# Optimization experiments

Hardware: AMD Instinct MI355X
Metric: run time of the kernel (lower is better)

Reference implementation:

```python
import jax, jax.numpy as jnp
import numpy as np

B, H, W, DIM, HEADS, WS = 32, 56, 56, 192, 6, 7
KD = DIM // HEADS          # key_dim = head_dim = 32 (attn_ratio=1.0 -> d = KD, dh = DIM)
DH = KD * HEADS
HQKV = DH + 2 * KD * HEADS # 576
L = H * W
HIDDEN = 4 * DIM
NWIN = (H // WS) * (W // WS)
NTOK = WS * WS
SCALE = KD ** -0.5


def _bias_idxs(ws):
    pts = [(i, j) for i in range(ws) for j in range(ws)]
    offs, idxs = {}, []
    for p1 in pts:
        for p2 in pts:
            o = (abs(p1[0] - p2[0]), abs(p1[1] - p2[1]))
            if o not in offs:
                offs[o] = len(offs)
            idxs.append(offs[o])
    return np.asarray(idxs, np.int32).reshape(ws * ws, ws * ws), len(offs)

BIAS_IDX, NOFF = _bias_idxs(WS)  # [49,49], 49 distinct offsets


def _ln(x, g, b, eps=1e-5):
    m = x.mean(-1, keepdims=True)
    v = jnp.mean((x - m) ** 2, -1, keepdims=True)
    return (x - m) * jax.lax.rsqrt(v + eps) * g + b


def setup_inputs() -> dict:
    key = jax.random.key(0)
    ks = jax.random.split(key, 8)
    f32 = jnp.float32
    return {
        "x": jax.random.normal(ks[0], (B, L, DIM), f32),
        "ln1_g": jnp.ones((DIM,), f32), "ln1_b": jnp.zeros((DIM,), f32),
        "qkv_w": jax.random.normal(ks[1], (DIM, HQKV), f32) * 0.02,
        "qkv_b": jnp.zeros((HQKV,), f32),
        "proj_w": jax.random.normal(ks[2], (DH, DIM), f32) * 0.02,
        "proj_b": jnp.zeros((DIM,), f32),
        "attn_bias": jax.random.normal(ks[3], (HEADS, NOFF), f32) * 0.02,
        "conv_w": jax.random.normal(ks[4], (DIM, 1, 3, 3), f32) * 0.1,  # depthwise OIHW
        "bn_g": jnp.ones((DIM,), f32), "bn_b": jnp.zeros((DIM,), f32),
        "bn_m": jnp.zeros((DIM,), f32), "bn_v": jnp.ones((DIM,), f32),
        "ln2_g": jnp.ones((DIM,), f32), "ln2_b": jnp.zeros((DIM,), f32),
        "fc1_w": jax.random.normal(ks[5], (DIM, HIDDEN), f32) * 0.02,
        "fc1_b": jnp.zeros((HIDDEN,), f32),
        "fc2_w": jax.random.normal(ks[6], (HIDDEN, DIM), f32) * 0.02,
        "fc2_b": jnp.zeros((DIM,), f32),
    }


def reference(x, ln1_g, ln1_b, qkv_w, qkv_b, proj_w, proj_b, attn_bias,
              conv_w, bn_g, bn_b, bn_m, bn_v, ln2_g, ln2_b,
              fc1_w, fc1_b, fc2_w, fc2_b):
    # ---- window partition: [B,L,C] -> [B*nWin, 49, C] (H,W divisible by WS, no pad)
    xw = x.reshape(B, H // WS, WS, W // WS, WS, DIM)
    xw = xw.transpose(0, 1, 3, 2, 4, 5).reshape(B * NWIN, NTOK, DIM)
    # ---- attention (pre-LN inside Attention module)
    h = _ln(xw, ln1_g, ln1_b)
    qkv = (h @ qkv_w + qkv_b).reshape(B * NWIN, NTOK, HEADS, 3 * KD)
    qkv = qkv.transpose(0, 2, 1, 3)                      # [Bw, heads, N, 3*KD]
    q, k, v = qkv[..., :KD], qkv[..., KD:2 * KD], qkv[..., 2 * KD:]
    bias = attn_bias[:, BIAS_IDX]                        # [heads, 49, 49] gathered table
    scores = jnp.einsum('bhnd,bhmd->bhnm', q, k) * SCALE + bias[None]
    a = jax.nn.softmax(scores, axis=-1)
    o = jnp.einsum('bhnm,bhmd->bhnd', a, v)
    o = o.transpose(0, 2, 1, 3).reshape(B * NWIN, NTOK, DH)
    o = o @ proj_w + proj_b
    # ---- window unpartition -> [B,L,C], residual add
    o = o.reshape(B, H // WS, W // WS, WS, WS, DIM)
    o = o.transpose(0, 1, 3, 2, 4, 5).reshape(B, L, DIM)
    x = x + o
    # ---- depthwise 3x3 conv + BN (eval-mode) in NCHW
    xc = x.transpose(0, 2, 1).reshape(B, DIM, H, W)
    xc = jax.lax.conv_general_dilated(
        xc, conv_w, window_strides=(1, 1), padding=[(1, 1), (1, 1)],
        feature_group_count=DIM, dimension_numbers=('NCHW', 'OIHW', 'NCHW'))
    inv = jax.lax.rsqrt(bn_v + 1e-5)
    xc = (xc - bn_m[None, :, None, None]) * (inv * bn_g)[None, :, None, None] + bn_b[None, :, None, None]
    x = xc.reshape(B, DIM, L).transpose(0, 2, 1)
    # ---- MLP (LN -> fc1 -> GELU(exact) -> fc2) with residual
    h2 = _ln(x, ln2_g, ln2_b)
    h2 = jax.nn.gelu(h2 @ fc1_w + fc1_b, approximate=False)
    h2 = h2 @ fc2_w + fc2_b
    return x + h2
```

## Files before the change

kernel.cpp:

```cpp
#include <hip/hip_runtime.h>
#include <hip/hip_bf16.h>

#define DIMC 192
#define LTOT 3136

using bf16x8 = __attribute__((ext_vector_type(8))) short;
using f32x4  = __attribute__((ext_vector_type(4))) float;

static __device__ __forceinline__ unsigned short f2bf(float f) {
  unsigned u = __builtin_bit_cast(unsigned, f);
  u = (u + 0x7FFFu + ((u >> 16) & 1u)) >> 16;
  return (unsigned short)u;
}
static __device__ __forceinline__ float bf2f(unsigned short u) {
  unsigned v = ((unsigned)u) << 16;
  return __builtin_bit_cast(float, v);
}
static __device__ __forceinline__ int iabs(int a) { return a < 0 ? -a : a; }

static __device__ __forceinline__ void gload16(const unsigned short* g, unsigned short* lds) {
  __builtin_amdgcn_global_load_lds(
      (const __attribute__((address_space(1))) void*)g,
      (__attribute__((address_space(3))) void*)lds, 16, 0, 0);
}

__global__ __launch_bounds__(256) void prep_k(
    const float* __restrict__ qkv_w, const float* __restrict__ proj_w,
    const float* __restrict__ fc1_w, const float* __restrict__ fc2_w,
    const float* __restrict__ conv_w,
    const float* __restrict__ bn_g, const float* __restrict__ bn_b,
    const float* __restrict__ bn_m, const float* __restrict__ bn_v,
    unsigned short* __restrict__ qkvT, unsigned short* __restrict__ projT,
    unsigned short* __restrict__ fc1T, unsigned short* __restrict__ fc2T,
    float* __restrict__ convT, float* __restrict__ bnsc, float* __restrict__ bnsh)
{
  int idx = blockIdx.x * 256 + threadIdx.x;
  if (idx < 122880) { int n = idx / 192, k = idx % 192;
    qkvT[idx] = (n < 576) ? f2bf(qkv_w[k * 576 + n]) : 0; return; }
  idx -= 122880;
  if (idx < 49152)  { int n = idx / 192, k = idx % 192;
    projT[idx] = (n < 192) ? f2bf(proj_w[k * 192 + n]) : 0; return; }
  idx -= 49152;
  if (idx < 147456) { int n = idx / 192, k = idx % 192;
    fc1T[idx] = f2bf(fc1_w[k * 768 + n]); return; }
  idx -= 147456;
  if (idx < 196608) { int n = idx / 768, k = idx % 768;
    fc2T[idx] = (n < 192) ? f2bf(fc2_w[k * 192 + n]) : 0; return; }
  idx -= 196608;
  if (idx < 1728)   { int tap = idx / 192, c = idx % 192; convT[idx] = conv_w[c * 9 + tap]; return; }
  idx -= 1728;
  if (idx < 192) {
    float s = bn_g[idx] * rsqrtf(bn_v[idx] + 1e-5f);
    bnsc[idx] = s; bnsh[idx] = bn_b[idx] - bn_m[idx] * s;
  }
}

__global__ __launch_bounds__(256) void ln1_k(
    const float* __restrict__ x, const float* __restrict__ g,
    const float* __restrict__ b, unsigned short* __restrict__ h1)
{
  const int grp = threadIdx.x >> 6, l = threadIdx.x & 63;
  const int m = blockIdx.x * 4 + grp;
  const int w = m / 49, t = m % 49;
  const int bb = w >> 6, win = w & 63;
  const int lpix = ((win >> 3) * 7 + t / 7) * 56 + (win & 7) * 7 + t % 7;
  const float* row = x + ((size_t)bb * LTOT + lpix) * DIMC;
  const bool act = l < 48;
  const int c = l * 4;
  float4 v = make_float4(0.f, 0.f, 0.f, 0.f);
  if (act) v = *(const float4*)(row + c);
  float s = v.x + v.y + v.z + v.w;
  float ss = v.x * v.x + v.y * v.y + v.z * v.z + v.w * v.w;
  #pragma unroll
  for (int off = 1; off < 64; off <<= 1) { s += __shfl_xor(s, off); ss += __shfl_xor(ss, off); }
  float mean = s * (1.f / 192.f);
  float rstd = rsqrtf(ss * (1.f / 192.f) - mean * mean + 1e-5f);
  if (act) {
    float4 gg = *(const float4*)(g + c);
    float4 bv = *(const float4*)(b + c);
    ushort4 o;
    o.x = f2bf((v.x - mean) * rstd * gg.x + bv.x);
    o.y = f2bf((v.y - mean) * rstd * gg.y + bv.y);
    o.z = f2bf((v.z - mean) * rstd * gg.z + bv.z);
    o.w = f2bf((v.w - mean) * rstd * gg.w + bv.w);
    *(ushort4*)(h1 + (size_t)m * DIMC + c) = o;
  }
}

__global__ __launch_bounds__(256) void qkvg_k(
    const unsigned short* __restrict__ h1, const unsigned short* __restrict__ qkvT,
    const float* __restrict__ qkv_b, unsigned short* __restrict__ qkv)
{
  __shared__ unsigned short Wc[12288];
  const int tid = threadIdx.x;
  const int l = tid & 63, wv = tid >> 6;
  const int u = l >> 4, ll = l & 15;
  const int m0 = blockIdx.x * 64;

  bf16x8 areg[6];
  {
    const unsigned short* arow = h1 + (size_t)(m0 + wv * 16 + ll) * 192;
    #pragma unroll
    for (int kk = 0; kk < 6; ++kk)
      areg[kk] = *(const bf16x8*)(arow + kk * 32 + u * 8);
  }
  for (int c = 0; c < 9; ++c) {
    if (c) __syncthreads();
    const char* Wg = (const char*)(qkvT + (size_t)c * 64 * 192);
    #pragma unroll
    for (int i = 0; i < 6; ++i) {
      int ob = i * 4096 + tid * 16;
      int r = ob / 384, cc = ob % 384;
      int cs = cc ^ ((r & 7) << 4);
      gload16((const unsigned short*)(Wg + r * 384 + cs), &Wc[ob >> 1]);
    }
    __syncthreads();
    f32x4 p1[4] = {};
    #pragma unroll
    for (int kk = 0; kk < 6; ++kk) {
      int cb = (kk * 64 + u * 16) ^ ((ll & 7) << 4);
      #pragma unroll
      for (int nf = 0; nf < 4; ++nf) {
        bf16x8 bfr = *(const bf16x8*)((const char*)Wc + (nf * 16 + ll) * 384 + cb);
        p1[nf] = __builtin_amdgcn_mfma_f32_16x16x32_bf16(areg[kk], bfr, p1[nf], 0, 0, 0);
      }
    }
    #pragma unroll
    for (int nf = 0; nf < 4; ++nf)
    #pragma unroll
    for (int r = 0; r < 4; ++r) {
      int m = m0 + wv * 16 + u * 4 + r;
      int n = c * 64 + nf * 16 + ll;
      qkv[(size_t)m * 576 + n] = f2bf(p1[nf][r] + qkv_b[n]);
    }
  }
}

__global__ __launch_bounds__(256) void attnp_k(
    const unsigned short* __restrict__ qkv, const float* __restrict__ attn_bias,
    const unsigned short* __restrict__ projT, const float* __restrict__ proj_b,
    const float* __restrict__ x, unsigned short* __restrict__ x1b)
{
  __shared__ unsigned short Qs[2560];
  __shared__ unsigned short Ks[2560];
  __shared__ unsigned short Vt[2304];
  __shared__ unsigned short Ps[4608];
  __shared__ float bias_s[52];
  const int tid = threadIdx.x;
  const int l = tid & 63, wv = tid >> 6;
  const int u = l >> 4, ll = l & 15;
  const int w = blockIdx.x, b = w >> 6, win = w & 63;
  const f32x4 fz = {0.f, 0.f, 0.f, 0.f};

  for (int i = tid; i < 15 * 40; i += 256) {
    Qs[(49 + i / 40) * 40 + i % 40] = 0;
    Ks[(49 + i / 40) * 40 + i % 40] = 0;
  }
  for (int i = tid; i < 32 * 15; i += 256) Vt[(i / 15) * 72 + 49 + i % 15] = 0;

  f32x4 pacc[4][3] = {};

  for (int h = 0; h < 6; ++h) {
    __syncthreads();
    if (tid < 49) bias_s[tid] = attn_bias[h * 49 + tid];
    #pragma unroll
    for (int it = 0; it < 3; ++it) {
      int idx = tid + it * 256;
      if (idx < 588) {
        int row = idx / 12, g = idx % 12;
        int4 v = *(const int4*)&qkv[((size_t)w * 49 + row) * 576 + h * 96 + g * 8];
        if (g < 4) *(int4*)&Qs[row * 40 + g * 8] = v;
        else if (g < 8) *(int4*)&Ks[row * 40 + (g - 4) * 8] = v;
        else {
          union { int4 v4; unsigned short us[8]; } uu; uu.v4 = v;
          int d0 = (g - 8) * 8;
          #pragma unroll
          for (int e = 0; e < 8; ++e) Vt[(d0 + e) * 72 + row] = uu.us[e];
        }
      }
    }
    __syncthreads();

    {
      const int qr = wv * 16 + ll;
      const int qi = qr > 48 ? 48 : qr;
      bf16x8 qf = *(const bf16x8*)&Qs[(wv * 16 + ll) * 40 + u * 8];
      f32x4 sc[4];
      #pragma unroll
      for (int kt = 0; kt < 4; ++kt) {
        bf16x8 kf = *(const bf16x8*)&Ks[(kt * 16 + ll) * 40 + u * 8];
        sc[kt] = __builtin_amdgcn_mfma_f32_16x16x32_bf16(kf, qf, fz, 0, 0, 0);
      }
      float sv[4][4];
      float mx = -1e30f;
      #pragma unroll
      for (int kt = 0; kt < 4; ++kt)
        #pragma unroll
        for (int r = 0; r < 4; ++r) {
          int kr = kt * 16 + u * 4 + r;
          float val = -1e30f;
          if (kr < 49)
            val = sc[kt][r] * 0.17677669529663689f +
                  bias_s[iabs(qi / 7 - kr / 7) * 7 + iabs(qi % 7 - kr % 7)];
          sv[kt][r] = val;
          mx = fmaxf(mx, val);
        }
      mx = fmaxf(mx, __shfl_xor(mx, 16));
      mx = fmaxf(mx, __shfl_xor(mx, 32));
      float sum = 0.f;
      #pragma unroll
      for (int kt = 0; kt < 4; ++kt)
        #pragma unroll
        for (int r = 0; r < 4; ++r) {
          float p = __expf(sv[kt][r] - mx);
          sv[kt][r] = p; sum += p;
        }
      sum += __shfl_xor(sum, 16);
      sum += __shfl_xor(sum, 32);
      float inv = 1.f / sum;
      #pragma unroll
      for (int kt = 0; kt < 4; ++kt)
        #pragma unroll
        for (int r = 0; r < 4; ++r)
          Ps[(wv * 16 + ll) * 72 + kt * 16 + u * 4 + r] = f2bf(sv[kt][r] * inv);
    }
    __syncthreads();

    {
      f32x4 oa[2] = {fz, fz};
      #pragma unroll
      for (int kk = 0; kk < 2; ++kk) {
        bf16x8 pf = *(const bf16x8*)&Ps[(wv * 16 + ll) * 72 + kk * 32 + u * 8];
        #pragma unroll
        for (int nt = 0; nt < 2; ++nt) {
          bf16x8 vf = *(const bf16x8*)&Vt[(nt * 16 + ll) * 72 + kk * 32 + u * 8];
          oa[nt] = __builtin_amdgcn_mfma_f32_16x16x32_bf16(pf, vf, oa[nt], 0, 0, 0);
        }
      }
      #pragma unroll
      for (int nt = 0; nt < 2; ++nt)
        #pragma unroll
        for (int r = 0; r < 4; ++r)
          Qs[(wv * 16 + u * 4 + r) * 40 + nt * 16 + ll] = f2bf(oa[nt][r]);
    }
    __syncthreads();

    {
      bf16x8 af[4], bfr[3];
      #pragma unroll
      for (int mt = 0; mt < 4; ++mt)
        af[mt] = *(const bf16x8*)&Qs[(mt * 16 + ll) * 40 + u * 8];
      #pragma unroll
      for (int nf = 0; nf < 3; ++nf)
        bfr[nf] = *(const bf16x8*)&projT[(size_t)(wv * 48 + nf * 16 + ll) * 192 + h * 32 + u * 8];
      #pragma unroll
      for (int mt = 0; mt < 4; ++mt)
        #pragma unroll
        for (int nf = 0; nf < 3; ++nf)
          pacc[mt][nf] = __builtin_amdgcn_mfma_f32_16x16x32_bf16(af[mt], bfr[nf], pacc[mt][nf], 0, 0, 0);
    }
  }

  #pragma unroll
  for (int mt = 0; mt < 4; ++mt)
  #pragma unroll
  for (int r = 0; r < 4; ++r) {
    int m = mt * 16 + u * 4 + r;
    if (m < 49) {
      int lpix = ((win >> 3) * 7 + m / 7) * 56 + (win & 7) * 7 + m % 7;
      size_t base = ((size_t)b * LTOT + lpix) * DIMC;
      #pragma unroll
      for (int nf = 0; nf < 3; ++nf) {
        int n = wv * 48 + nf * 16 + ll;
        float val = pacc[mt][nf][r] + proj_b[n] + x[base + n];
        x1b[base + n] = f2bf(val);
      }
    }
  }
}

__global__ __launch_bounds__(256) void fmlp_k(
    const unsigned short* __restrict__ h2, const unsigned short* __restrict__ fc1T,
    const float* __restrict__ fc1_b, const unsigned short* __restrict__ fc2T,
    const float* __restrict__ fc2_b, const unsigned short* __restrict__ x2,
    float* __restrict__ out)
{
  __shared__ unsigned short W1[12288];
  __shared__ unsigned short P[4096];
  const int tid = threadIdx.x;
  const int l = tid & 63, wv = tid >> 6;
  const int u = l >> 4, ll = l & 15;
  const int m0 = blockIdx.x * 64;
  f32x4 acc[4][3] = {};

  bf16x8 areg[6];
  {
    const unsigned short* arow = h2 + (size_t)(m0 + wv * 16 + ll) * 192;
    #pragma unroll
    for (int kk = 0; kk < 6; ++kk)
      areg[kk] = *(const bf16x8*)(arow + kk * 32 + u * 8);
  }

  for (int c = 0; c < 12; ++c) {
    __syncthreads();
    const char* W1g = (const char*)(fc1T + (size_t)c * 64 * 192);
    #pragma unroll
    for (int i = 0; i < 6; ++i) {
      int ob = i * 4096 + tid * 16;
      int r = ob / 384, cc = ob % 384;
      int cs = cc ^ ((r & 7) << 4);
      gload16((const unsigned short*)(W1g + r * 384 + cs), &W1[ob >> 1]);
    }
    bf16x8 b2r[2][3];
    #pragma unroll
    for (int kk = 0; kk < 2; ++kk)
      #pragma unroll
      for (int nf = 0; nf < 3; ++nf)
        b2r[kk][nf] = *(const bf16x8*)&fc2T[(size_t)(wv * 48 + nf * 16 + ll) * 768 + c * 64 + kk * 32 + u * 8];
    __syncthreads();
    {
      f32x4 p1[4] = {};
      #pragma unroll
      for (int kk = 0; kk < 6; ++kk) {
        int cb = (kk * 64 + u * 16) ^ ((ll & 7) << 4);
        #pragma unroll
        for (int nf = 0; nf < 4; ++nf) {
          bf16x8 bfr = *(const bf16x8*)((const char*)W1 + (nf * 16 + ll) * 384 + cb);
          p1[nf] = __builtin_amdgcn_mfma_f32_16x16x32_bf16(areg[kk], bfr, p1[nf], 0, 0, 0);
        }
      }
      #pragma unroll
      for (int nf = 0; nf < 4; ++nf)
      #pragma unroll
      for (int r = 0; r < 4; ++r) {
        int mrow = wv * 16 + u * 4 + r;
        int n = nf * 16 + ll;
        float v = p1[nf][r] + fc1_b[c * 64 + n];
        float gl = v / (1.f + __expf(-1.5957691216057308f * (v + 0.044715f * v * v * v)));
        *(unsigned short*)((char*)P + mrow * 128 + ((n * 2) ^ ((mrow & 7) << 4))) = f2bf(gl);
      }
    }
    __syncthreads();
    #pragma unroll
    for (int kk = 0; kk < 2; ++kk) {
      int cb = kk * 64 + u * 16;
      #pragma unroll
      for (int mt = 0; mt < 4; ++mt) {
        bf16x8 af2 = *(const bf16x8*)((const char*)P + (mt * 16 + ll) * 128 + (cb ^ ((ll & 7) << 4)));
        #pragma unroll
        for (int nf = 0; nf < 3; ++nf)
          acc[mt][nf] = __builtin_amdgcn_mfma_f32_16x16x32_bf16(af2, b2r[kk][nf], acc[mt][nf], 0, 0, 0);
      }
    }
  }
  #pragma unroll
  for (int mt = 0; mt < 4; ++mt)
  #pragma unroll
  for (int r = 0; r < 4; ++r) {
    int m = m0 + mt * 16 + u * 4 + r;
    #pragma unroll
    for (int nf = 0; nf < 3; ++nf) {
      int n = wv * 48 + nf * 16 + ll;
      size_t o = (size_t)m * 192 + n;
      out[o] = acc[mt][nf][r] + fc2_b[n] + bf2f(x2[o]);
    }
  }
}

__global__ __launch_bounds__(256) void conv_k(
    const unsigned short* __restrict__ x1b, const float* __restrict__ wT,
    const float* __restrict__ bnsc, const float* __restrict__ bnsh,
    const float* __restrict__ g2, const float* __restrict__ b2,
    unsigned short* __restrict__ x2, unsigned short* __restrict__ h2)
{
  const int bid = blockIdx.x;
  const int swz = (bid & 7) * 3136 + (bid >> 3);
  const int grp = threadIdx.x >> 6, l = threadIdx.x & 63;
  const int gid = swz * 4 + grp;
  const int b = gid / LTOT, p = gid % LTOT;
  const int i = p / 56, j = p % 56;
  const bool act = l < 48;
  const int c = l * 4;
  float4 acc = make_float4(0.f, 0.f, 0.f, 0.f);
  if (act) {
    #pragma unroll
    for (int di = -1; di <= 1; ++di) {
      int ni = i + di;
      if (ni < 0 || ni >= 56) continue;
      #pragma unroll
      for (int dj = -1; dj <= 1; ++dj) {
        int nj = j + dj;
        if (nj < 0 || nj >= 56) continue;
        ushort4 sv = *(const ushort4*)&x1b[((size_t)b * LTOT + ni * 56 + nj) * DIMC + c];
        float4 wv = *(const float4*)&wT[((di + 1) * 3 + (dj + 1)) * DIMC + c];
        acc.x += bf2f(sv.x) * wv.x; acc.y += bf2f(sv.y) * wv.y;
        acc.z += bf2f(sv.z) * wv.z; acc.w += bf2f(sv.w) * wv.w;
      }
    }
    float4 s4 = *(const float4*)&bnsc[c];
    float4 h4 = *(const float4*)&bnsh[c];
    acc.x = acc.x * s4.x + h4.x; acc.y = acc.y * s4.y + h4.y;
    acc.z = acc.z * s4.z + h4.z; acc.w = acc.w * s4.w + h4.w;
    ushort4 xv;
    xv.x = f2bf(acc.x); xv.y = f2bf(acc.y); xv.z = f2bf(acc.z); xv.w = f2bf(acc.w);
    *(ushort4*)&x2[(size_t)gid * DIMC + c] = xv;
  }
  float s = act ? acc.x + acc.y + acc.z + acc.w : 0.f;
  float ss = act ? acc.x * acc.x + acc.y * acc.y + acc.z * acc.z + acc.w * acc.w : 0.f;
  #pragma unroll
  for (int off = 1; off < 64; off <<= 1) { s += __shfl_xor(s, off); ss += __shfl_xor(ss, off); }
  float mean = s * (1.f / 192.f);
  float rstd = rsqrtf(ss * (1.f / 192.f) - mean * mean + 1e-5f);
  if (act) {
    float4 gg = *(const float4*)&g2[c];
    float4 bb = *(const float4*)&b2[c];
    ushort4 ov;
    ov.x = f2bf((acc.x - mean) * rstd * gg.x + bb.x);
    ov.y = f2bf((acc.y - mean) * rstd * gg.y + bb.y);
    ov.z = f2bf((acc.z - mean) * rstd * gg.z + bb.z);
    ov.w = f2bf((acc.w - mean) * rstd * gg.w + bb.w);
    *(ushort4*)&h2[(size_t)gid * DIMC + c] = ov;
  }
}

extern "C" void kernel_launch(void* const* d_in, const int* in_sizes, int n_in,
                              void* d_out, int out_size, void* d_ws, size_t ws_size,
                              hipStream_t stream) {
  const float* x      = (const float*)d_in[0];
  const float* ln1_g  = (const float*)d_in[1];
  const float* ln1_b  = (const float*)d_in[2];
  const float* qkv_w  = (const float*)d_in[3];
  const float* qkv_b  = (const float*)d_in[4];
  const float* proj_w = (const float*)d_in[5];
  const float* proj_b = (const float*)d_in[6];
  const float* attn_b = (const float*)d_in[7];
  const float* conv_w = (const float*)d_in[8];
  const float* bn_g   = (const float*)d_in[9];
  const float* bn_b   = (const float*)d_in[10];
  const float* bn_m   = (const float*)d_in[11];
  const float* bn_v   = (const float*)d_in[12];
  const float* ln2_g  = (const float*)d_in[13];
  const float* ln2_b  = (const float*)d_in[14];
  const float* fc1_w  = (const float*)d_in[15];
  const float* fc1_b  = (const float*)d_in[16];
  const float* fc2_w  = (const float*)d_in[17];
  const float* fc2_b  = (const float*)d_in[18];
  float* out = (float*)d_out;

  const size_t AOFF = 1048576, BOFF = AOFF + 115605504;
  const size_t NEEDED = BOFF + 38535168;
  if (ws_size < NEEDED) return;

  char* ws = (char*)d_ws;
  unsigned short* qkvT  = (unsigned short*)(ws);
  unsigned short* projT = (unsigned short*)(ws + 245760);
  unsigned short* fc1T  = (unsigned short*)(ws + 344064);
  unsigned short* fc2T  = (unsigned short*)(ws + 638976);
  float*          convT = (float*)(ws + 1032192);
  float*          bnsc  = (float*)(ws + 1039104);
  float*          bnsh  = (float*)(ws + 1039872);

  unsigned short* qkv = (unsigned short*)(ws + AOFF);
  unsigned short* x2  = (unsigned short*)(ws + AOFF);
  unsigned short* h2  = (unsigned short*)(ws + AOFF + 38535168);
  unsigned short* h1  = (unsigned short*)(ws + BOFF);
  unsigned short* x1b = (unsigned short*)(ws + BOFF);

  prep_k<<<2024, 256, 0, stream>>>(qkv_w, proj_w, fc1_w, fc2_w, conv_w,
                                   bn_g, bn_b, bn_m, bn_v,
                                   qkvT, projT, fc1T, fc2T, convT, bnsc, bnsh);
  ln1_k<<<25088, 256, 0, stream>>>(x, ln1_g, ln1_b, h1);
  qkvg_k<<<1568, 256, 0, stream>>>(h1, qkvT, qkv_b, qkv);
  attnp_k<<<2048, 256, 0, stream>>>(qkv, attn_b, projT, proj_b, x, x1b);
  conv_k<<<25088, 256, 0, stream>>>(x1b, convT, bnsc, bnsh, ln2_g, ln2_b, x2, h2);
  fmlp_k<<<1568, 256, 0, stream>>>(h2, fc1T, fc1_b, fc2T, fc2_b, x2, out);
}
```

Before: 410.7 us.

## Stage fc2 weights in LDS and give each wave its own output rows

In the fused MLP kernel, the fc2 weight chunk for each hidden slice is now copied into a swizzled LDS buffer instead of being loaded per-wave from global memory into registers. The second GEMM is repartitioned so that each wave reads only its own 16 rows of the GELU tile P, which its own lanes wrote, and computes all 192 output columns. That removes the barrier between writing P and the fc2 MFMAs, and one barrier at loop start is skipped. The cost is 24KB more LDS per block, which may reduce occupancy, plus a synchronous global-to-LDS copy of W2 each iteration.

```diff
diff --git a/kernel.cpp b/kernel.cpp
--- a/kernel.cpp
+++ b/kernel.cpp
@@ -286,12 +286,13 @@
     float* __restrict__ out)
 {
   __shared__ unsigned short W1[12288];
+  __shared__ unsigned short W2[12288];
   __shared__ unsigned short P[4096];
   const int tid = threadIdx.x;
   const int l = tid & 63, wv = tid >> 6;
   const int u = l >> 4, ll = l & 15;
   const int m0 = blockIdx.x * 64;
-  f32x4 acc[4][3] = {};
+  f32x4 acc[12] = {};
 
   bf16x8 areg[6];
   {
@@ -302,7 +303,7 @@
   }
 
   for (int c = 0; c < 12; ++c) {
-    __syncthreads();
+    if (c) __syncthreads();
     const char* W1g = (const char*)(fc1T + (size_t)c * 64 * 192);
     #pragma unroll
     for (int i = 0; i < 6; ++i) {
@@ -311,13 +312,15 @@
       int cs = cc ^ ((r & 7) << 4);
       gload16((const unsigned short*)(W1g + r * 384 + cs), &W1[ob >> 1]);
     }
-    bf16x8 b2r[2][3];
-    #pragma unroll
-    for (int kk = 0; kk < 2; ++kk)
-      #pragma unroll
-      for (int nf = 0; nf < 3; ++nf)
-        b2r[kk][nf] = *(const bf16x8*)&fc2T[(size_t)(wv * 48 + nf * 16 + ll) * 768 + c * 64 + kk * 32 + u * 8];
-    __syncthreads();
+    #pragma unroll
+    for (int i = 0; i < 6; ++i) {
+      int unit = i * 256 + tid;
+      int r = unit >> 3, q = unit & 7;
+      int4 vv = *(const int4*)&fc2T[(size_t)r * 768 + c * 64 + q * 8];
+      *(int4*)((char*)W2 + r * 128 + ((q * 16) ^ ((r & 7) << 4))) = vv;
+    }
+    __syncthreads();
+
     {
       f32x4 p1[4] = {};
       #pragma unroll
@@ -340,30 +343,31 @@
         *(unsigned short*)((char*)P + mrow * 128 + ((n * 2) ^ ((mrow & 7) << 4))) = f2bf(gl);
       }
     }
-    __syncthreads();
-    #pragma unroll
-    for (int kk = 0; kk < 2; ++kk) {
-      int cb = kk * 64 + u * 16;
-      #pragma unroll
-      for (int mt = 0; mt < 4; ++mt) {
-        bf16x8 af2 = *(const bf16x8*)((const char*)P + (mt * 16 + ll) * 128 + (cb ^ ((ll & 7) << 4)));
-        #pragma unroll
-        for (int nf = 0; nf < 3; ++nf)
-          acc[mt][nf] = __builtin_amdgcn_mfma_f32_16x16x32_bf16(af2, b2r[kk][nf], acc[mt][nf], 0, 0, 0);
-      }
-    }
-  }
-  #pragma unroll
-  for (int mt = 0; mt < 4; ++mt)
+    {
+      bf16x8 af2[2];
+      #pragma unroll
+      for (int kk = 0; kk < 2; ++kk)
+        af2[kk] = *(const bf16x8*)((const char*)P + (wv * 16 + ll) * 128 +
+                                   ((kk * 64 + u * 16) ^ ((ll & 7) << 4)));
+      #pragma unroll
+      for (int nt = 0; nt < 12; ++nt) {
+        #pragma unroll
+        for (int kk = 0; kk < 2; ++kk) {
+          bf16x8 bfr = *(const bf16x8*)((const char*)W2 + (nt * 16 + ll) * 128 +
+                                        ((kk * 64 + u * 16) ^ ((ll & 7) << 4)));
+          acc[nt] = __builtin_amdgcn_mfma_f32_16x16x32_bf16(af2[kk], bfr, acc[nt], 0, 0, 0);
+        }
+      }
+    }
+  }
+  #pragma unroll
+  for (int nt = 0; nt < 12; ++nt)
   #pragma unroll
   for (int r = 0; r < 4; ++r) {
-    int m = m0 + mt * 16 + u * 4 + r;
-    #pragma unroll
-    for (int nf = 0; nf < 3; ++nf) {
-      int n = wv * 48 + nf * 16 + ll;
-      size_t o = (size_t)m * 192 + n;
-      out[o] = acc[mt][nf][r] + fc2_b[n] + bf2f(x2[o]);
-    }
+    int m = m0 + wv * 16 + u * 4 + r;
+    int n = nt * 16 + ll;
+    size_t o = (size_t)m * 192 + n;
+    out[o] = acc[nt][r] + fc2_b[n] + bf2f(x2[o]);
   }
 }
 
```

New measurement: 385.9 us. 1.06x faster.
